# Kernel tuning notes

Hardware: AMD Instinct MI355X
Metric: run time of the kernel (lower is better)

## Reference

```python
import jax, jax.numpy as jnp
import numpy as np


def setup_inputs() -> dict:
    key = jax.random.key(0)
    ks = jax.random.split(key, 6)
    B, F, E, H, U = 64, 4096, 256, 512, 512
    scale = 0.02
    return {
        "features": jax.random.normal(ks[0], (B, F, E), dtype=jnp.float32),
        "hidden": jax.random.normal(ks[1], (B, H), dtype=jnp.float32),
        "W1_w": jax.random.normal(ks[2], (E, U), dtype=jnp.float32) * scale,
        "W1_b": jnp.zeros((U,), dtype=jnp.float32),
        "W2_w": jax.random.normal(ks[3], (H, U), dtype=jnp.float32) * scale,
        "W2_b": jnp.zeros((U,), dtype=jnp.float32),
        "V_w": jax.random.normal(ks[4], (U, 1), dtype=jnp.float32) * scale,
        "V_b": jnp.zeros((1,), dtype=jnp.float32),
    }


def reference(features, hidden, W1_w, W1_b, W2_w, W2_b, V_w, V_b):
    # features: (B, F, E); hidden: (B, H)
    proj_f = jnp.einsum("bfe,eu->bfu", features, W1_w) + W1_b          # (B, F, U)
    proj_h = (hidden @ W2_w + W2_b)[:, None, :]                        # (B, 1, U)
    attention_hidden = jnp.tanh(proj_f + proj_h)                       # (B, F, U)
    scores = jnp.einsum("bfu,uo->bfo", attention_hidden, V_w) + V_b    # (B, F, 1)
    attention_weights = jax.nn.softmax(scores, axis=1)                 # (B, F, 1)
    context_vector = jnp.sum(attention_weights * features, axis=1)     # (B, E)
    return (context_vector, attention_weights)
```

## Files before the change

### kernel.cpp

```cpp
#include <hip/hip_runtime.h>
#include <cmath>

constexpr int Bdim = 64;
constexpr int Fdim = 4096;
constexpr int Edim = 256;
constexpr int Hdim = 512;
constexpr int Udim = 512;

typedef __attribute__((ext_vector_type(8))) short short8;
typedef __attribute__((ext_vector_type(4))) float f32x4;

__device__ __forceinline__ unsigned short f2bf(float f) {
    unsigned int u = __float_as_uint(f);
    u += 0x7FFFu + ((u >> 16) & 1u);
    return (unsigned short)(u >> 16);
}
__device__ __forceinline__ unsigned int pack2(float lo, float hi) {
    return (unsigned int)f2bf(lo) | ((unsigned int)f2bf(hi) << 16);
}
__device__ __forceinline__ float tanh_fast(float x) {
    float e = __expf(2.0f * x);
    return 1.0f - 2.0f * __builtin_amdgcn_rcpf(e + 1.0f);
}
__device__ __forceinline__ void gload_lds16(const void* g, void* l) {
    __builtin_amdgcn_global_load_lds(
        (const __attribute__((address_space(1))) unsigned int*)g,
        (__attribute__((address_space(3))) unsigned int*)l, 16, 0, 0);
}

__global__ __launch_bounds__(256) void prep_kernel(
    const float* __restrict__ hidden, const float* __restrict__ W2,
    const float* __restrict__ W1b, const float* __restrict__ W2b,
    float* __restrict__ cb,
    const float* __restrict__ W1, unsigned short* __restrict__ Th,
    float* __restrict__ ctx, const int do_t)
{
    const int bid = blockIdx.x;
    const int tid = threadIdx.x;

    if (bid < 128) {
        const int b = bid >> 1;
        const int u = (bid & 1) * 256 + tid;
        const float* hb = hidden + (size_t)b * Hdim;
        float acc = 0.f;
        #pragma unroll 8
        for (int h = 0; h < Hdim; ++h)
            acc = fmaf(hb[h], W2[(size_t)h * Udim + u], acc);
        cb[(size_t)b * Udim + u] = acc + W1b[u] + W2b[u];
    } else if (bid < 160) {
        if (!do_t) return;
        __shared__ unsigned short sT[64][72];
        const int k  = bid - 128;
        const int e0 = (k & 3) * 64, u0 = (k >> 2) * 64;
        const int ue = tid & 63, er = tid >> 6;
        #pragma unroll
        for (int it = 0; it < 16; ++it) {
            const int e = er + it * 4;
            sT[ue][e] = f2bf(W1[(size_t)(e0 + e) * Udim + u0 + ue]);
        }
        __syncthreads();
        const int ur = tid >> 2, cq = tid & 3;
        const int u = u0 + ur, s = u & 7;
        const int cA = (e0 >> 3) + cq * 2;
        uint4 a  = *(const uint4*)&sT[ur][cq * 16];
        uint4 b2 = *(const uint4*)&sT[ur][cq * 16 + 8];
        unsigned short* dst = Th + (size_t)u * Edim;
        *(uint4*)(dst + ((cA ^ s) << 3))       = a;
        *(uint4*)(dst + (((cA + 1) ^ s) << 3)) = b2;
    } else {
        const int idx = (bid - 160) * 256 + tid;
        ((float4*)ctx)[idx] = make_float4(0.f, 0.f, 0.f, 0.f);
    }
}

__global__ __launch_bounds__(256, 2) void score_mfma4_kernel(
    const float* __restrict__ feat,
    const unsigned short* __restrict__ W1Ts,
    const float* __restrict__ Vw, const float* __restrict__ Vb,
    const float* __restrict__ cb, float* __restrict__ scores)
{
    __shared__ unsigned short lds[16896];

    const int b    = blockIdx.y;
    const int f0   = blockIdx.x * 128;
    const int tid  = threadIdx.x;
    const int lane = tid & 63;
    const int w    = tid >> 6;
    const int ln15 = lane & 15;
    const int kq   = lane >> 4;
    const int swz  = ln15 & 7;

    short8 af[2][8];
    {
        unsigned short* sAw = lds + w * 4224;
        const float* gA = feat + ((size_t)(b * Fdim + f0 + w * 32)) * Edim;
        #pragma unroll
        for (int h = 0; h < 2; ++h) {
            #pragma unroll
            for (int r = 0; r < 16; ++r) {
                float4 v = *(const float4*)(gA + (size_t)(h * 16 + r) * Edim + lane * 4);
                uint2 p; p.x = pack2(v.x, v.y); p.y = pack2(v.z, v.w);
                *(uint2*)&sAw[r * 264 + lane * 4] = p;
            }
            #pragma unroll
            for (int k8 = 0; k8 < 8; ++k8)
                af[h][k8] = *(const short8*)&sAw[ln15 * 264 + k8 * 32 + kq * 8];
        }
    }
    __syncthreads();

    float sacc[2][4] = {};
    const float* cbB = cb + (size_t)b * Udim;

    {
        const char* gB = (const char*)W1Ts;
        #pragma unroll
        for (int t = 0; t < 4; ++t) {
            const int chunk = w * 4 + t;
            gload_lds16(gB + (size_t)chunk * 1024 + lane * 16,
                        (char*)lds + chunk * 1024);
        }
    }
    __syncthreads();

    for (int p = 0; p < 16; ++p) {
        if (p < 15) {
            const char* gB = (const char*)(W1Ts + (size_t)(p + 1) * 32 * Edim);
            char* lb = (char*)lds + ((p + 1) & 1) * 16384;
            #pragma unroll
            for (int t = 0; t < 4; ++t) {
                const int chunk = w * 4 + t;
                gload_lds16(gB + (size_t)chunk * 1024 + lane * 16,
                            lb + chunk * 1024);
            }
        }

        const unsigned short* bw = lds + (p & 1) * 8192;
        const int ub = p * 32;
        const float cu0 = cbB[ub + ln15],     cu1 = cbB[ub + 16 + ln15];
        const float vv0 = Vw[ub + ln15],      vv1 = Vw[ub + 16 + ln15];
        f32x4 acc[2][2] = {};
        #pragma unroll
        for (int k8 = 0; k8 < 8; ++k8) {
            const int co = ((k8 * 4 + kq) ^ swz) * 8;
            short8 b0 = *(const short8*)&bw[ln15 * 256 + co];
            short8 b1 = *(const short8*)&bw[(16 + ln15) * 256 + co];
            #pragma unroll
            for (int mi = 0; mi < 2; ++mi) {
                acc[mi][0] = __builtin_amdgcn_mfma_f32_16x16x32_bf16(
                    af[mi][k8], b0, acc[mi][0], 0, 0, 0);
                acc[mi][1] = __builtin_amdgcn_mfma_f32_16x16x32_bf16(
                    af[mi][k8], b1, acc[mi][1], 0, 0, 0);
            }
        }
        #pragma unroll
        for (int mi = 0; mi < 2; ++mi)
            #pragma unroll
            for (int r = 0; r < 4; ++r)
                sacc[mi][r] += tanh_fast(acc[mi][0][r] + cu0) * vv0
                             + tanh_fast(acc[mi][1][r] + cu1) * vv1;

        if (p < 15) __syncthreads();
    }

    const float vb = Vb[0];
    #pragma unroll
    for (int mi = 0; mi < 2; ++mi)
        #pragma unroll
        for (int r = 0; r < 4; ++r) {
            float s = sacc[mi][r];
            s += __shfl_xor(s, 1);
            s += __shfl_xor(s, 2);
            s += __shfl_xor(s, 4);
            s += __shfl_xor(s, 8);
            if (ln15 == 0)
                scores[(size_t)b * Fdim + f0 + w * 32 + mi * 16 + kq * 4 + r] = s + vb;
        }
}

constexpr int TFt = 64;
constexpr int TUt = 64;
constexpr int LDR = Edim + 4;

__global__ __launch_bounds__(256) void score_kernel(
    const float* __restrict__ feat, const float* __restrict__ W1,
    const float* __restrict__ Vw, const float* __restrict__ Vb,
    const float* __restrict__ cb, float* __restrict__ scores)
{
    __shared__ float sA[TFt * LDR];
    __shared__ float sW[TUt * LDR];

    const int b   = blockIdx.y;
    const int f0  = blockIdx.x * TFt;
    const int tid = threadIdx.x;
    const int tf  = tid >> 4;
    const int tu  = tid & 15;

    {
        const float4* gA = (const float4*)(feat + ((size_t)b * Fdim + f0) * Edim);
        #pragma unroll
        for (int it = 0; it < 16; ++it) {
            const int i = tid + it * 256;
            const int f = i >> 6;
            const int qq = i & 63;
            const float4 v = gA[i];
            *(float4*)&sA[f * LDR + 4 * qq] = v;
        }
    }

    float sacc[4] = {0.f, 0.f, 0.f, 0.f};
    const float* cbb = cb + (size_t)b * Udim;

    for (int uc = 0; uc < Udim; uc += TUt) {
        __syncthreads();
        #pragma unroll
        for (int it = 0; it < 16; ++it) {
            const int i = tid + it * 256;
            const int e = i >> 4;
            const int qq = i & 15;
            const float4 v = *(const float4*)(W1 + (size_t)e * Udim + uc + 4 * qq);
            sW[(4 * qq + 0) * LDR + e] = v.x;
            sW[(4 * qq + 1) * LDR + e] = v.y;
            sW[(4 * qq + 2) * LDR + e] = v.z;
            sW[(4 * qq + 3) * LDR + e] = v.w;
        }
        __syncthreads();

        float acc[4][4] = {};
        #pragma unroll 4
        for (int e = 0; e < Edim; e += 4) {
            float4 a0 = *(const float4*)&sA[(tf +  0) * LDR + e];
            float4 a1 = *(const float4*)&sA[(tf + 16) * LDR + e];
            float4 a2 = *(const float4*)&sA[(tf + 32) * LDR + e];
            float4 a3 = *(const float4*)&sA[(tf + 48) * LDR + e];
            float4 w0 = *(const float4*)&sW[(tu +  0) * LDR + e];
            float4 w1 = *(const float4*)&sW[(tu + 16) * LDR + e];
            float4 w2 = *(const float4*)&sW[(tu + 32) * LDR + e];
            float4 w3 = *(const float4*)&sW[(tu + 48) * LDR + e];
            #define FMA4(i, j, A, W)                         \
                acc[i][j] = fmaf(A.x, W.x, acc[i][j]);       \
                acc[i][j] = fmaf(A.y, W.y, acc[i][j]);       \
                acc[i][j] = fmaf(A.z, W.z, acc[i][j]);       \
                acc[i][j] = fmaf(A.w, W.w, acc[i][j]);
            FMA4(0,0,a0,w0) FMA4(0,1,a0,w1) FMA4(0,2,a0,w2) FMA4(0,3,a0,w3)
            FMA4(1,0,a1,w0) FMA4(1,1,a1,w1) FMA4(1,2,a1,w2) FMA4(1,3,a1,w3)
            FMA4(2,0,a2,w0) FMA4(2,1,a2,w1) FMA4(2,2,a2,w2) FMA4(2,3,a2,w3)
            FMA4(3,0,a3,w0) FMA4(3,1,a3,w1) FMA4(3,2,a3,w2) FMA4(3,3,a3,w3)
            #undef FMA4
        }

        #pragma unroll
        for (int j = 0; j < 4; ++j) {
            const int u = uc + tu + 16 * j;
            const float vw = Vw[u];
            const float cuv = cbb[u];
            #pragma unroll
            for (int i = 0; i < 4; ++i)
                sacc[i] = fmaf(tanhf(acc[i][j] + cuv), vw, sacc[i]);
        }
    }

    const float vb = Vb[0];
    #pragma unroll
    for (int i = 0; i < 4; ++i) {
        float s = sacc[i];
        s += __shfl_xor(s, 1);
        s += __shfl_xor(s, 2);
        s += __shfl_xor(s, 4);
        s += __shfl_xor(s, 8);
        if (tu == 0)
            scores[(size_t)b * Fdim + f0 + tf + 16 * i] = s + vb;
    }
}

__global__ __launch_bounds__(256) void softmax_stats_kernel(
    const float* __restrict__ sc, float2* __restrict__ st)
{
    __shared__ float red[8];
    const int b   = blockIdx.x;
    const int tid = threadIdx.x;
    const float* row = sc + (size_t)b * Fdim;

    float v[16];
    float m = -INFINITY;
    #pragma unroll
    for (int i = 0; i < 16; ++i) {
        v[i] = row[tid + 256 * i];
        m = fmaxf(m, v[i]);
    }
    #pragma unroll
    for (int off = 1; off < 64; off <<= 1)
        m = fmaxf(m, __shfl_xor(m, off));
    if ((tid & 63) == 0) red[tid >> 6] = m;
    __syncthreads();
    m = fmaxf(fmaxf(red[0], red[1]), fmaxf(red[2], red[3]));

    float s = 0.f;
    #pragma unroll
    for (int i = 0; i < 16; ++i)
        s += expf(v[i] - m);
    #pragma unroll
    for (int off = 1; off < 64; off <<= 1)
        s += __shfl_xor(s, off);
    if ((tid & 63) == 0) red[4 + (tid >> 6)] = s;
    __syncthreads();
    if (tid == 0) {
        const float tot = red[4] + red[5] + red[6] + red[7];
        st[b] = make_float2(m, 1.0f / tot);
    }
}

__global__ __launch_bounds__(256) void ctxnorm_kernel(
    const float* __restrict__ feat, const float2* __restrict__ st,
    float* __restrict__ wts, float* __restrict__ ctx)
{
    __shared__ float  wl[256];
    __shared__ float4 sred[256];

    const int b   = blockIdx.y;
    const int f0  = blockIdx.x * 256;
    const int tid = threadIdx.x;

    const float2 s2 = st[b];
    const size_t wix = (size_t)b * Fdim + f0 + tid;
    const float wgt = expf(wts[wix] - s2.x) * s2.y;
    wts[wix] = wgt;
    wl[tid]  = wgt;
    __syncthreads();

    const int e4 = tid & 63;
    const int fg = tid >> 6;
    const float4* fp = (const float4*)(feat + ((size_t)b * Fdim + f0) * Edim);

    float4 a = make_float4(0.f, 0.f, 0.f, 0.f);
    #pragma unroll 8
    for (int i = 0; i < 64; ++i) {
        const int f = i * 4 + fg;
        const float4 v = fp[(size_t)f * 64 + e4];
        const float wv = wl[f];
        a.x = fmaf(wv, v.x, a.x);
        a.y = fmaf(wv, v.y, a.y);
        a.z = fmaf(wv, v.z, a.z);
        a.w = fmaf(wv, v.w, a.w);
    }
    sred[tid] = a;
    __syncthreads();

    if (fg == 0) {
        const float4 r0 = sred[e4];
        const float4 r1 = sred[64 + e4];
        const float4 r2 = sred[128 + e4];
        const float4 r3 = sred[192 + e4];
        float* cp = ctx + (size_t)b * Edim + e4 * 4;
        atomicAdd(cp + 0, r0.x + r1.x + r2.x + r3.x);
        atomicAdd(cp + 1, r0.y + r1.y + r2.y + r3.y);
        atomicAdd(cp + 2, r0.z + r1.z + r2.z + r3.z);
        atomicAdd(cp + 3, r0.w + r1.w + r2.w + r3.w);
    }
}

extern "C" void kernel_launch(void* const* d_in, const int* in_sizes, int n_in,
                              void* d_out, int out_size, void* d_ws, size_t ws_size,
                              hipStream_t stream)
{
    const float* features = (const float*)d_in[0];
    const float* hidden   = (const float*)d_in[1];
    const float* W1w      = (const float*)d_in[2];
    const float* W1b      = (const float*)d_in[3];
    const float* W2w      = (const float*)d_in[4];
    const float* W2b      = (const float*)d_in[5];
    const float* Vw       = (const float*)d_in[6];
    const float* Vb       = (const float*)d_in[7];

    float* ctx = (float*)d_out;
    float* wts = (float*)d_out + (size_t)Bdim * Edim;

    float*  cb    = (float*)d_ws;
    float2* stats = (float2*)((char*)d_ws + 131072);
    unsigned short* W1Ts = (unsigned short*)((char*)d_ws + 131584);
    const size_t NEED = 131584 + (size_t)Udim * Edim * 2;
    const int mfma_ok = (ws_size >= NEED) ? 1 : 0;

    prep_kernel<<<176, 256, 0, stream>>>(hidden, W2w, W1b, W2b, cb,
                                         W1w, W1Ts, ctx, mfma_ok);

    if (mfma_ok) {
        dim3 sgrid(Fdim / 128, Bdim);
        score_mfma4_kernel<<<sgrid, 256, 0, stream>>>(features, W1Ts, Vw, Vb, cb, wts);
    } else {
        dim3 sgrid(Fdim / TFt, Bdim);
        score_kernel<<<sgrid, 256, 0, stream>>>(features, W1w, Vw, Vb, cb, wts);
    }

    softmax_stats_kernel<<<Bdim, 256, 0, stream>>>(wts, stats);

    dim3 cgrid(Fdim / 256, Bdim);
    ctxnorm_kernel<<<cgrid, 256, 0, stream>>>(features, stats, wts, ctx);
}
```

Before: 480.4 us.

## Fuse softmax stats into context kernel and shrink score tile for occupancy

The score kernel now processes 64 feature rows per block instead of 128, one 16-row M-tile per wave, and declares launch bounds of 4 blocks per SM to raise occupancy. Raw scores go to a workspace buffer. The separate softmax-stats kernel is removed: each context block recomputes the row max and sum from that buffer before normalising and accumulating its slice. This saves a launch and a dependent pass, at the cost of every block re-reading its 16 KB score row and the W1 tiles being streamed twice as often. The fallback path gets separate softmax and context kernels.

After: 481.3 us. No clear change (+0.2%).

```diff
diff --git a/kernel.cpp b/kernel.cpp
--- a/kernel.cpp
+++ b/kernel.cpp
@@ -73,16 +73,16 @@
     }
 }
 
-__global__ __launch_bounds__(256, 2) void score_mfma4_kernel(
+__global__ __launch_bounds__(256, 4) void score_mfma4_kernel(
     const float* __restrict__ feat,
     const unsigned short* __restrict__ W1Ts,
     const float* __restrict__ Vw, const float* __restrict__ Vb,
-    const float* __restrict__ cb, float* __restrict__ scores)
+    const float* __restrict__ cb, float* __restrict__ scr)
 {
     __shared__ unsigned short lds[16896];
 
     const int b    = blockIdx.y;
-    const int f0   = blockIdx.x * 128;
+    const int f0   = blockIdx.x * 64;
     const int tid  = threadIdx.x;
     const int lane = tid & 63;
     const int w    = tid >> 6;
@@ -90,26 +90,23 @@
     const int kq   = lane >> 4;
     const int swz  = ln15 & 7;
 
-    short8 af[2][8];
+    short8 af[8];
     {
         unsigned short* sAw = lds + w * 4224;
-        const float* gA = feat + ((size_t)(b * Fdim + f0 + w * 32)) * Edim;
-        #pragma unroll
-        for (int h = 0; h < 2; ++h) {
-            #pragma unroll
-            for (int r = 0; r < 16; ++r) {
-                float4 v = *(const float4*)(gA + (size_t)(h * 16 + r) * Edim + lane * 4);
-                uint2 p; p.x = pack2(v.x, v.y); p.y = pack2(v.z, v.w);
-                *(uint2*)&sAw[r * 264 + lane * 4] = p;
-            }
-            #pragma unroll
-            for (int k8 = 0; k8 < 8; ++k8)
-                af[h][k8] = *(const short8*)&sAw[ln15 * 264 + k8 * 32 + kq * 8];
-        }
-    }
-    __syncthreads();
-
-    float sacc[2][4] = {};
+        const float* gA = feat + ((size_t)(b * Fdim + f0 + w * 16)) * Edim;
+        #pragma unroll
+        for (int r = 0; r < 16; ++r) {
+            float4 v = *(const float4*)(gA + (size_t)r * Edim + lane * 4);
+            uint2 p; p.x = pack2(v.x, v.y); p.y = pack2(v.z, v.w);
+            *(uint2*)&sAw[r * 264 + lane * 4] = p;
+        }
+        #pragma unroll
+        for (int k8 = 0; k8 < 8; ++k8)
+            af[k8] = *(const short8*)&sAw[ln15 * 264 + k8 * 32 + kq * 8];
+    }
+    __syncthreads();
+
+    float sacc[4] = {};
     const float* cbB = cb + (size_t)b * Udim;
 
     {
@@ -139,43 +136,109 @@
         const int ub = p * 32;
         const float cu0 = cbB[ub + ln15],     cu1 = cbB[ub + 16 + ln15];
         const float vv0 = Vw[ub + ln15],      vv1 = Vw[ub + 16 + ln15];
-        f32x4 acc[2][2] = {};
+        f32x4 acc0 = {}, acc1 = {};
         #pragma unroll
         for (int k8 = 0; k8 < 8; ++k8) {
             const int co = ((k8 * 4 + kq) ^ swz) * 8;
             short8 b0 = *(const short8*)&bw[ln15 * 256 + co];
             short8 b1 = *(const short8*)&bw[(16 + ln15) * 256 + co];
-            #pragma unroll
-            for (int mi = 0; mi < 2; ++mi) {
-                acc[mi][0] = __builtin_amdgcn_mfma_f32_16x16x32_bf16(
-                    af[mi][k8], b0, acc[mi][0], 0, 0, 0);
-                acc[mi][1] = __builtin_amdgcn_mfma_f32_16x16x32_bf16(
-                    af[mi][k8], b1, acc[mi][1], 0, 0, 0);
-            }
-        }
-        #pragma unroll
-        for (int mi = 0; mi < 2; ++mi)
-            #pragma unroll
-            for (int r = 0; r < 4; ++r)
-                sacc[mi][r] += tanh_fast(acc[mi][0][r] + cu0) * vv0
-                             + tanh_fast(acc[mi][1][r] + cu1) * vv1;
+            acc0 = __builtin_amdgcn_mfma_f32_16x16x32_bf16(af[k8], b0, acc0, 0, 0, 0);
+            acc1 = __builtin_amdgcn_mfma_f32_16x16x32_bf16(af[k8], b1, acc1, 0, 0, 0);
+        }
+        #pragma unroll
+        for (int r = 0; r < 4; ++r)
+            sacc[r] += tanh_fast(acc0[r] + cu0) * vv0
+                     + tanh_fast(acc1[r] + cu1) * vv1;
 
         if (p < 15) __syncthreads();
     }
 
     const float vb = Vb[0];
     #pragma unroll
-    for (int mi = 0; mi < 2; ++mi)
-        #pragma unroll
-        for (int r = 0; r < 4; ++r) {
-            float s = sacc[mi][r];
-            s += __shfl_xor(s, 1);
-            s += __shfl_xor(s, 2);
-            s += __shfl_xor(s, 4);
-            s += __shfl_xor(s, 8);
-            if (ln15 == 0)
-                scores[(size_t)b * Fdim + f0 + w * 32 + mi * 16 + kq * 4 + r] = s + vb;
-        }
+    for (int r = 0; r < 4; ++r) {
+        float s = sacc[r];
+        s += __shfl_xor(s, 1);
+        s += __shfl_xor(s, 2);
+        s += __shfl_xor(s, 4);
+        s += __shfl_xor(s, 8);
+        if (ln15 == 0)
+            scr[(size_t)b * Fdim + f0 + w * 16 + kq * 4 + r] = s + vb;
+    }
+}
+
+__global__ __launch_bounds__(256) void ctxnorm_kernel(
+    const float* __restrict__ feat, const float* __restrict__ scr,
+    float* __restrict__ wts, float* __restrict__ ctx)
+{
+    __shared__ float  red[8];
+    __shared__ float  wl[256];
+    __shared__ float4 sred[256];
+
+    const int b   = blockIdx.y;
+    const int fc  = blockIdx.x;
+    const int f0  = fc * 256;
+    const int tid = threadIdx.x;
+    const float* row = scr + (size_t)b * Fdim;
+
+    float v[16];
+    float m = -INFINITY;
+    #pragma unroll
+    for (int i = 0; i < 16; ++i) {
+        v[i] = row[tid + 256 * i];
+        m = fmaxf(m, v[i]);
+    }
+    #pragma unroll
+    for (int off = 1; off < 64; off <<= 1)
+        m = fmaxf(m, __shfl_xor(m, off));
+    if ((tid & 63) == 0) red[tid >> 6] = m;
+    __syncthreads();
+    m = fmaxf(fmaxf(red[0], red[1]), fmaxf(red[2], red[3]));
+
+    float s = 0.f;
+    #pragma unroll
+    for (int i = 0; i < 16; ++i)
+        s += expf(v[i] - m);
+    #pragma unroll
+    for (int off = 1; off < 64; off <<= 1)
+        s += __shfl_xor(s, off);
+    if ((tid & 63) == 0) red[4 + (tid >> 6)] = s;
+    __syncthreads();
+    const float inv = 1.0f / (red[4] + red[5] + red[6] + red[7]);
+
+    const float wgt = expf(v[fc] - m) * inv;
+    wts[(size_t)b * Fdim + f0 + tid] = wgt;
+    wl[tid] = wgt;
+    __syncthreads();
+
+    const int e4 = tid & 63;
+    const int fg = tid >> 6;
+    const float4* fp = (const float4*)(feat + ((size_t)b * Fdim + f0) * Edim);
+
+    float4 a = make_float4(0.f, 0.f, 0.f, 0.f);
+    #pragma unroll 8
+    for (int i = 0; i < 64; ++i) {
+        const int f = i * 4 + fg;
+        const float4 fv = fp[(size_t)f * 64 + e4];
+        const float wv = wl[f];
+        a.x = fmaf(wv, fv.x, a.x);
+        a.y = fmaf(wv, fv.y, a.y);
+        a.z = fmaf(wv, fv.z, a.z);
+        a.w = fmaf(wv, fv.w, a.w);
+    }
+    sred[tid] = a;
+    __syncthreads();
+
+    if (fg == 0) {
+        const float4 r0 = sred[e4];
+        const float4 r1 = sred[64 + e4];
+        const float4 r2 = sred[128 + e4];
+        const float4 r3 = sred[192 + e4];
+        float* cp = ctx + (size_t)b * Edim + e4 * 4;
+        atomicAdd(cp + 0, r0.x + r1.x + r2.x + r3.x);
+        atomicAdd(cp + 1, r0.y + r1.y + r2.y + r3.y);
+        atomicAdd(cp + 2, r0.z + r1.z + r2.z + r3.z);
+        atomicAdd(cp + 3, r0.w + r1.w + r2.w + r3.w);
+    }
 }
 
 constexpr int TFt = 64;
@@ -273,13 +336,12 @@
     }
 }
 
-__global__ __launch_bounds__(256) void softmax_stats_kernel(
-    const float* __restrict__ sc, float2* __restrict__ st)
-{
-    __shared__ float red[8];
-    const int b   = blockIdx.x;
+__global__ __launch_bounds__(256) void softmax_kernel(float* __restrict__ sc)
+{
+    __shared__ float red[256];
+    const int b = blockIdx.x;
     const int tid = threadIdx.x;
-    const float* row = sc + (size_t)b * Fdim;
+    float* row = sc + (size_t)b * Fdim;
 
     float v[16];
     float m = -INFINITY;
@@ -288,75 +350,50 @@
         v[i] = row[tid + 256 * i];
         m = fmaxf(m, v[i]);
     }
-    #pragma unroll
-    for (int off = 1; off < 64; off <<= 1)
-        m = fmaxf(m, __shfl_xor(m, off));
-    if ((tid & 63) == 0) red[tid >> 6] = m;
-    __syncthreads();
-    m = fmaxf(fmaxf(red[0], red[1]), fmaxf(red[2], red[3]));
-
-    float s = 0.f;
+    red[tid] = m;
+    __syncthreads();
+    for (int s = 128; s > 0; s >>= 1) {
+        if (tid < s) red[tid] = fmaxf(red[tid], red[tid + s]);
+        __syncthreads();
+    }
+    m = red[0];
+    __syncthreads();
+
+    float sum = 0.f;
+    #pragma unroll
+    for (int i = 0; i < 16; ++i) {
+        v[i] = expf(v[i] - m);
+        sum += v[i];
+    }
+    red[tid] = sum;
+    __syncthreads();
+    for (int s = 128; s > 0; s >>= 1) {
+        if (tid < s) red[tid] += red[tid + s];
+        __syncthreads();
+    }
+    const float inv = 1.f / red[0];
     #pragma unroll
     for (int i = 0; i < 16; ++i)
-        s += expf(v[i] - m);
-    #pragma unroll
-    for (int off = 1; off < 64; off <<= 1)
-        s += __shfl_xor(s, off);
-    if ((tid & 63) == 0) red[4 + (tid >> 6)] = s;
-    __syncthreads();
-    if (tid == 0) {
-        const float tot = red[4] + red[5] + red[6] + red[7];
-        st[b] = make_float2(m, 1.0f / tot);
-    }
-}
-
-__global__ __launch_bounds__(256) void ctxnorm_kernel(
-    const float* __restrict__ feat, const float2* __restrict__ st,
-    float* __restrict__ wts, float* __restrict__ ctx)
-{
-    __shared__ float  wl[256];
-    __shared__ float4 sred[256];
-
-    const int b   = blockIdx.y;
-    const int f0  = blockIdx.x * 256;
-    const int tid = threadIdx.x;
-
-    const float2 s2 = st[b];
-    const size_t wix = (size_t)b * Fdim + f0 + tid;
-    const float wgt = expf(wts[wix] - s2.x) * s2.y;
-    wts[wix] = wgt;
-    wl[tid]  = wgt;
-    __syncthreads();
-
-    const int e4 = tid & 63;
-    const int fg = tid >> 6;
-    const float4* fp = (const float4*)(feat + ((size_t)b * Fdim + f0) * Edim);
-
-    float4 a = make_float4(0.f, 0.f, 0.f, 0.f);
+        row[tid + 256 * i] = v[i] * inv;
+}
+
+__global__ __launch_bounds__(256) void context_kernel(
+    const float* __restrict__ feat, const float* __restrict__ wts,
+    float* __restrict__ ctx)
+{
+    const int b  = blockIdx.y;
+    const int fc = blockIdx.x;
+    const int e  = threadIdx.x;
+
+    const float* fp = feat + ((size_t)b * Fdim + (size_t)fc * 256) * Edim + e;
+    const float* wp = wts + (size_t)b * Fdim + (size_t)fc * 256;
+
+    float acc = 0.f;
     #pragma unroll 8
-    for (int i = 0; i < 64; ++i) {
-        const int f = i * 4 + fg;
-        const float4 v = fp[(size_t)f * 64 + e4];
-        const float wv = wl[f];
-        a.x = fmaf(wv, v.x, a.x);
-        a.y = fmaf(wv, v.y, a.y);
-        a.z = fmaf(wv, v.z, a.z);
-        a.w = fmaf(wv, v.w, a.w);
-    }
-    sred[tid] = a;
-    __syncthreads();
-
-    if (fg == 0) {
-        const float4 r0 = sred[e4];
-        const float4 r1 = sred[64 + e4];
-        const float4 r2 = sred[128 + e4];
-        const float4 r3 = sred[192 + e4];
-        float* cp = ctx + (size_t)b * Edim + e4 * 4;
-        atomicAdd(cp + 0, r0.x + r1.x + r2.x + r3.x);
-        atomicAdd(cp + 1, r0.y + r1.y + r2.y + r3.y);
-        atomicAdd(cp + 2, r0.z + r1.z + r2.z + r3.z);
-        atomicAdd(cp + 3, r0.w + r1.w + r2.w + r3.w);
-    }
+    for (int f = 0; f < 256; ++f)
+        acc = fmaf(wp[f], fp[(size_t)f * Edim], acc);
+
+    atomicAdd(&ctx[(size_t)b * Edim + e], acc);
 }
 
 extern "C" void kernel_launch(void* const* d_in, const int* in_sizes, int n_in,
@@ -375,25 +412,25 @@
     float* ctx = (float*)d_out;
     float* wts = (float*)d_out + (size_t)Bdim * Edim;
 
-    float*  cb    = (float*)d_ws;
-    float2* stats = (float2*)((char*)d_ws + 131072);
-    unsigned short* W1Ts = (unsigned short*)((char*)d_ws + 131584);
-    const size_t NEED = 131584 + (size_t)Udim * Edim * 2;
+    float*          cb   = (float*)d_ws;
+    unsigned short* W1Ts = (unsigned short*)((char*)d_ws + 131072);
+    float*          scr  = (float*)((char*)d_ws + 131072 + 262144);
+    const size_t NEED = 131072 + 262144 + (size_t)Bdim * Fdim * sizeof(float);
     const int mfma_ok = (ws_size >= NEED) ? 1 : 0;
 
     prep_kernel<<<176, 256, 0, stream>>>(hidden, W2w, W1b, W2b, cb,
                                          W1w, W1Ts, ctx, mfma_ok);
 
     if (mfma_ok) {
-        dim3 sgrid(Fdim / 128, Bdim);
-        score_mfma4_kernel<<<sgrid, 256, 0, stream>>>(features, W1Ts, Vw, Vb, cb, wts);
+        dim3 sgrid(Fdim / 64, Bdim);
+        score_mfma4_kernel<<<sgrid, 256, 0, stream>>>(features, W1Ts, Vw, Vb, cb, scr);
+        dim3 cgrid(Fdim / 256, Bdim);
+        ctxnorm_kernel<<<cgrid, 256, 0, stream>>>(features, scr, wts, ctx);
     } else {
         dim3 sgrid(Fdim / TFt, Bdim);
         score_kernel<<<sgrid, 256, 0, stream>>>(features, W1w, Vw, Vb, cb, wts);
-    }
-
-    softmax_stats_kernel<<<Bdim, 256, 0, stream>>>(wts, stats);
-
-    dim3 cgrid(Fdim / 256, Bdim);
-    ctxnorm_kernel<<<cgrid, 256, 0, stream>>>(features, stats, wts, ctx);
-}
+        softmax_kernel<<<Bdim, 256, 0, stream>>>(wts);
+        dim3 cgrid(16, Bdim);
+        context_kernel<<<cgrid, 256, 0, stream>>>(features, wts, ctx);
+    }
+}
```
